# Kernel tuning notes

Hardware: AMD Instinct MI355X
Metric: run time of the kernel (lower is better)

The kernel has to match this reference:

```python
import jax, jax.numpy as jnp
import numpy as np

V = 50000        # output_size (vocab)
H = 1024         # internal hidden = hidden_size*2
L = 400          # max_length (encoder length)
B = 64
OOV_PAD = 500


def setup_inputs() -> dict:
    key = jax.random.key(0)
    ks = jax.random.split(key, 16)
    s = 0.02
    inp = {
        "input_ids": jax.random.randint(ks[0], (B,), 0, V),
        "hidden": jax.random.normal(ks[1], (1, B, H), jnp.float32),
        "encoder_outputs": jax.random.normal(ks[2], (L, B, H), jnp.float32),
        "full_input": jax.random.randint(ks[3], (B, L), 0, V),
        # parameters
        "emb": jax.random.normal(ks[4], (V, H), jnp.float32) * s,
        "attn_W": jax.random.normal(ks[5], (L, 2 * H), jnp.float32) * s,
        "attn_b": jnp.zeros((L,), jnp.float32),
        "comb_W": jax.random.normal(ks[6], (H, 2 * H), jnp.float32) * s,
        "comb_b": jnp.zeros((H,), jnp.float32),
        "W_ih": jax.random.normal(ks[7], (3 * H, H), jnp.float32) * s,
        "W_hh": jax.random.normal(ks[8], (3 * H, H), jnp.float32) * s,
        "b_ih": jnp.zeros((3 * H,), jnp.float32),
        "b_hh": jnp.zeros((3 * H,), jnp.float32),
        "out_W": jax.random.normal(ks[9], (V, H), jnp.float32) * s,
        "out_b": jnp.zeros((V,), jnp.float32),
        "gen_W": jax.random.normal(ks[10], (1, 2 * H), jnp.float32) * s,
        "gen_b": jnp.zeros((1,), jnp.float32),
    }
    return inp


def _decoder_step(input_ids, hidden, encoder_outputs, full_input,
                  emb, attn_W, attn_b, comb_W, comb_b,
                  W_ih, W_hh, b_ih, b_hh, out_W, out_b, gen_W, gen_b):
    embedded = emb[input_ids]                      # [B,H] (dropout is eval-mode identity)
    h0 = hidden[0]                                 # [B,H]

    # attention over fixed max_length positions
    cat = jnp.concatenate([embedded, h0], axis=1)  # [B,2H]
    attn_weights = jax.nn.softmax(cat @ attn_W.T + attn_b, axis=1)  # [B,L]
    enc = jnp.transpose(encoder_outputs, (1, 0, 2))                 # [B,L,H]
    attn_applied = jnp.einsum('bl,blh->bh', attn_weights, enc)      # [B,H]

    combined = jnp.concatenate([embedded, attn_applied], axis=1) @ comb_W.T + comb_b  # [B,H]

    # single-step GRU (PyTorch gate layout: r, z, n)
    gi = combined @ W_ih.T + b_ih
    gh = h0 @ W_hh.T + b_hh
    ir, iz, inn = jnp.split(gi, 3, axis=1)
    hr, hz, hn = jnp.split(gh, 3, axis=1)
    r = jax.nn.sigmoid(ir + hr)
    z = jax.nn.sigmoid(iz + hz)
    n = jnp.tanh(inn + r * hn)
    h_new = (1.0 - z) * n + z * h0                 # gru_output[0]

    p_vocab = jax.nn.log_softmax(h_new @ out_W.T + out_b, axis=1)   # [B,V]

    gen_in = jnp.concatenate([combined, h0], axis=1)                # [B,2H]
    p_gen = jax.nn.sigmoid(gen_in @ gen_W.T + gen_b)                # [B,1]

    # pointer copy distribution via scatter-add into [B, V+500]
    token_dist = jnp.zeros((input_ids.shape[0], V + OOV_PAD), p_vocab.dtype)
    rows = jnp.arange(input_ids.shape[0])[:, None]                  # [B,1]
    token_dist = token_dist.at[rows, full_input].add(attn_weights)

    p_vocab_scaled = p_vocab * p_gen
    padded = jnp.concatenate(
        [p_vocab_scaled, jnp.zeros((input_ids.shape[0], OOV_PAD), p_vocab.dtype)], axis=1)
    p_final = padded + (1.0 - p_gen) * token_dist
    # original module returns the INPUT hidden (not gru_hidden)
    return p_final, hidden, attn_weights


def reference(input_ids, hidden, encoder_outputs, full_input,
              emb, attn_W, attn_b, comb_W, comb_b,
              W_ih, W_hh, b_ih, b_hh, out_W, out_b, gen_W, gen_b):
    return _decoder_step(input_ids, hidden, encoder_outputs, full_input,
                         emb, attn_W, attn_b, comb_W, comb_b,
                         W_ih, W_hh, b_ih, b_hh, out_W, out_b, gen_W, gen_b)
```

## Files before the change

### kernel.cpp

```cpp
#include <hip/hip_runtime.h>
#include <cstddef>

#define B_ 64
#define H_ 1024
#define L_ 400
#define V_ 50000
#define VP_ 50500

typedef short short8 __attribute__((ext_vector_type(8)));
typedef float f32x4 __attribute__((ext_vector_type(4)));

static __device__ __forceinline__ short f2bf(float f) {
  unsigned u = __float_as_uint(f);
  u += 0x7fffu + ((u >> 16) & 1u);
  return (short)(u >> 16);
}

static __device__ __forceinline__ short8 pack8(float4 a, float4 b) {
  short8 r;
  r[0] = f2bf(a.x); r[1] = f2bf(a.y); r[2] = f2bf(a.z); r[3] = f2bf(a.w);
  r[4] = f2bf(b.x); r[5] = f2bf(b.y); r[6] = f2bf(b.z); r[7] = f2bf(b.w);
  return r;
}

__global__ void k_prep(const int* __restrict__ ids, const float* __restrict__ emb,
                       const float* __restrict__ hid, float* __restrict__ E,
                       float* __restrict__ A, float* __restrict__ hid_out) {
  int b = blockIdx.x;
  int t = threadIdx.x;
  int row = ids[b];
  float4 v = ((const float4*)(emb + (size_t)row * H_))[t];
  ((float4*)(E + (size_t)b * H_))[t] = v;
  ((float4*)(A + (size_t)b * H_))[t] = make_float4(0.f, 0.f, 0.f, 0.f);
  ((float4*)(hid_out + (size_t)b * H_))[t] = ((const float4*)(hid + (size_t)b * H_))[t];
}

__global__ __launch_bounds__(256) void k_gemm_small(
    const float* __restrict__ W0, const float* __restrict__ bias0,
    const float* __restrict__ Xa0, const float* __restrict__ Xb0,
    float* __restrict__ out0, int N0, int K0, int ldo0,
    const float* __restrict__ W1, const float* __restrict__ bias1,
    const float* __restrict__ Xa1, const float* __restrict__ Xb1,
    float* __restrict__ out1, int N1, int K1, int ldo1) {
  const float* W  = blockIdx.y ? W1  : W0;
  const float* bias = blockIdx.y ? bias1 : bias0;
  const float* Xa = blockIdx.y ? Xa1 : Xa0;
  const float* Xb = blockIdx.y ? Xb1 : Xb0;
  float* out = blockIdx.y ? out1 : out0;
  int N = blockIdx.y ? N1 : N0;
  int K = blockIdx.y ? K1 : K0;
  int ldo = blockIdx.y ? ldo1 : ldo0;

  int tid = threadIdx.x, wave = tid >> 6, lane = tid & 63;
  int q = lane >> 4, nl = lane & 15;
  int n = blockIdx.x * 16 + nl;
  int nld = n < N ? n : (N - 1);
  int kpw = K >> 2;
  int kbeg = wave * kpw;
  const float* wr = W + (size_t)nld * K;

  f32x4 acc[4];
  #pragma unroll
  for (int i = 0; i < 4; ++i) acc[i] = (f32x4){0.f, 0.f, 0.f, 0.f};

  for (int k0 = kbeg; k0 < kbeg + kpw; k0 += 32) {
    int kk = k0 + q * 8;
    float4 w0 = *(const float4*)(wr + kk);
    float4 w1 = *(const float4*)(wr + kk + 4);
    short8 bf = pack8(w0, w1);
    const float* Xsel = (kk < 1024) ? Xa : Xb;
    int kx = kk & 1023;
    #pragma unroll
    for (int mt = 0; mt < 4; ++mt) {
      const float* xp = Xsel + (size_t)(mt * 16 + nl) * H_ + kx;
      float4 x0 = *(const float4*)xp;
      float4 x1 = *(const float4*)(xp + 4);
      short8 af = pack8(x0, x1);
      acc[mt] = __builtin_amdgcn_mfma_f32_16x16x32_bf16(af, bf, acc[mt], 0, 0, 0);
    }
  }

  __shared__ float red[4][64][16];
  #pragma unroll
  for (int mt = 0; mt < 4; ++mt)
    #pragma unroll
    for (int r = 0; r < 4; ++r)
      red[wave][mt * 16 + q * 4 + r][nl] = acc[mt][r];
  __syncthreads();
  for (int i = tid; i < 1024; i += 256) {
    int m = i >> 4, c = i & 15;
    int nn = blockIdx.x * 16 + c;
    if (nn < N) {
      float s = red[0][m][c] + red[1][m][c] + red[2][m][c] + red[3][m][c] + bias[nn];
      out[(size_t)m * ldo + nn] = s;
    }
  }
}

__global__ __launch_bounds__(256) void k_attnsm(
    const float* __restrict__ S, const float* __restrict__ enc,
    float* __restrict__ aw_out, float* __restrict__ A) {
  __shared__ float w[L_];
  __shared__ float red[256];
  int lc = blockIdx.x, b = blockIdx.y, t = threadIdx.x;
  float a0 = S[b * L_ + t];
  float a1 = (t < L_ - 256) ? S[b * L_ + 256 + t] : -1e30f;
  float m = fmaxf(a0, a1);
  red[t] = m; __syncthreads();
  for (int s = 128; s > 0; s >>= 1) { if (t < s) red[t] = fmaxf(red[t], red[t + s]); __syncthreads(); }
  m = red[0]; __syncthreads();
  float e0 = __expf(a0 - m);
  float e1 = (t < L_ - 256) ? __expf(a1 - m) : 0.f;
  red[t] = e0 + e1; __syncthreads();
  for (int s = 128; s > 0; s >>= 1) { if (t < s) red[t] += red[t + s]; __syncthreads(); }
  float z = red[0];
  w[t] = e0 / z;
  if (t < L_ - 256) w[256 + t] = e1 / z;
  __syncthreads();
  if (lc == 0) {
    aw_out[b * L_ + t] = w[t];
    if (t < L_ - 256) aw_out[b * L_ + 256 + t] = w[256 + t];
  }
  float4 acc = make_float4(0.f, 0.f, 0.f, 0.f);
  for (int l = lc * 25; l < lc * 25 + 25; ++l) {
    float wg = w[l];
    float4 e = ((const float4*)(enc + ((size_t)l * B_ + b) * H_))[t];
    acc.x += wg * e.x; acc.y += wg * e.y; acc.z += wg * e.z; acc.w += wg * e.w;
  }
  float* dst = A + (size_t)b * H_ + t * 4;
  atomicAdd(dst + 0, acc.x); atomicAdd(dst + 1, acc.y);
  atomicAdd(dst + 2, acc.z); atomicAdd(dst + 3, acc.w);
}

__global__ __launch_bounds__(256) void k_gru_gen(
    const float* __restrict__ gi, const float* __restrict__ gh,
    const float* __restrict__ hid, short* __restrict__ HNb,
    const float* __restrict__ C, const float* __restrict__ gW,
    const float* __restrict__ gb, float* __restrict__ PG) {
  __shared__ float red[256];
  int blk = blockIdx.x, t = threadIdx.x;
  if (blk < 256) {
    int idx = blk * 256 + t;
    int b = idx >> 10, h = idx & 1023;
    float ir = gi[b * 3072 + h], iz = gi[b * 3072 + 1024 + h], inn = gi[b * 3072 + 2048 + h];
    float hr = gh[b * 3072 + h], hz = gh[b * 3072 + 1024 + h], hn = gh[b * 3072 + 2048 + h];
    float r = 1.f / (1.f + __expf(-(ir + hr)));
    float z = 1.f / (1.f + __expf(-(iz + hz)));
    float n = tanhf(inn + r * hn);
    HNb[idx] = f2bf((1.f - z) * n + z * hid[idx]);
  } else {
    int b = blk - 256;
    float acc = 0.f;
    for (int k = t; k < 2 * H_; k += 256) {
      float x = (k < H_) ? C[b * H_ + k] : hid[b * H_ + k - H_];
      acc += x * gW[k];
    }
    red[t] = acc; __syncthreads();
    for (int s = 128; s > 0; s >>= 1) { if (t < s) red[t] += red[t + s]; __syncthreads(); }
    if (t == 0) PG[b] = 1.f / (1.f + __expf(-(red[0] + gb[0])));
  }
}

__global__ __launch_bounds__(256) void k_gemm_vocab(
    const short* __restrict__ Xb, const float* __restrict__ W,
    const float* __restrict__ bias, float* __restrict__ P) {
  int tid = threadIdx.x, wave = tid >> 6, lane = tid & 63;
  int q = lane >> 4, nl = lane & 15;
  int n = blockIdx.x * 64 + wave * 16 + nl;
  int nld = n < V_ ? n : (V_ - 1);
  const float* wr = W + (size_t)nld * H_;
  f32x4 acc[4];
  #pragma unroll
  for (int i = 0; i < 4; ++i) acc[i] = (f32x4){0.f, 0.f, 0.f, 0.f};

  for (int k0 = 0; k0 < H_; k0 += 32) {
    int kk = k0 + q * 8;
    float4 w0 = *(const float4*)(wr + kk);
    float4 w1 = *(const float4*)(wr + kk + 4);
    short8 bf = pack8(w0, w1);
    #pragma unroll
    for (int mt = 0; mt < 4; ++mt) {
      short8 af = *(const short8*)(Xb + (size_t)(mt * 16 + nl) * H_ + kk);
      acc[mt] = __builtin_amdgcn_mfma_f32_16x16x32_bf16(af, bf, acc[mt], 0, 0, 0);
    }
  }
  if (n < V_) {
    float bv = bias[n];
    #pragma unroll
    for (int mt = 0; mt < 4; ++mt)
      #pragma unroll
      for (int r = 0; r < 4; ++r)
        P[(size_t)(mt * 16 + q * 4 + r) * VP_ + n] = acc[mt][r] + bv;
  }
}

__global__ __launch_bounds__(256) void k_rowred2(const float* __restrict__ P,
                                                 float* __restrict__ MX,
                                                 float* __restrict__ SE) {
  __shared__ float red[256];
  int b = blockIdx.x >> 2, c = blockIdx.x & 3;
  int t = threadIdx.x;
  int v0 = c * 12500, v1 = v0 + 12500;
  float m = -1e30f;
  for (int v = v0 + t; v < v1; v += 256) m = fmaxf(m, P[(size_t)b * VP_ + v]);
  red[t] = m; __syncthreads();
  for (int s = 128; s > 0; s >>= 1) { if (t < s) red[t] = fmaxf(red[t], red[t + s]); __syncthreads(); }
  m = red[0]; __syncthreads();
  float sum = 0.f;
  for (int v = v0 + t; v < v1; v += 256) sum += __expf(P[(size_t)b * VP_ + v] - m);
  red[t] = sum; __syncthreads();
  for (int s = 128; s > 0; s >>= 1) { if (t < s) red[t] += red[t + s]; __syncthreads(); }
  if (t == 0) { MX[blockIdx.x] = m; SE[blockIdx.x] = red[0]; }
}

__global__ void k_final(float* __restrict__ P, const float* __restrict__ pg,
                        const float* __restrict__ MX, const float* __restrict__ SE) {
  int b = blockIdx.y;
  float m0 = MX[b * 4], m1 = MX[b * 4 + 1], m2 = MX[b * 4 + 2], m3 = MX[b * 4 + 3];
  float M = fmaxf(fmaxf(m0, m1), fmaxf(m2, m3));
  float Z = SE[b * 4] * __expf(m0 - M) + SE[b * 4 + 1] * __expf(m1 - M)
          + SE[b * 4 + 2] * __expf(m2 - M) + SE[b * 4 + 3] * __expf(m3 - M);
  float lz = M + __logf(Z);
  float g = pg[b];
  int v0 = blockIdx.x * 1024 + threadIdx.x * 4;
  if (v0 >= VP_) return;
  float4* p = (float4*)(P + (size_t)b * VP_ + v0);
  if (v0 < V_) {
    float4 x = *p;
    x.x = g * (x.x - lz); x.y = g * (x.y - lz);
    x.z = g * (x.z - lz); x.w = g * (x.w - lz);
    *p = x;
  } else {
    *p = make_float4(0.f, 0.f, 0.f, 0.f);
  }
}

__global__ void k_scatter(float* __restrict__ P, const float* __restrict__ aw,
                          const int* __restrict__ fi, const float* __restrict__ pg) {
  int b = blockIdx.x, t = threadIdx.x;
  if (t >= L_) return;
  float g = 1.f - pg[b];
  int v = fi[b * L_ + t];
  atomicAdd(P + (size_t)b * VP_ + v, g * aw[b * L_ + t]);
}

extern "C" void kernel_launch(void* const* d_in, const int* in_sizes, int n_in,
                              void* d_out, int out_size, void* d_ws, size_t ws_size,
                              hipStream_t stream) {
  const int*   ids    = (const int*)d_in[0];
  const float* hid    = (const float*)d_in[1];
  const float* enc    = (const float*)d_in[2];
  const int*   fi     = (const int*)d_in[3];
  const float* emb    = (const float*)d_in[4];
  const float* attn_W = (const float*)d_in[5];
  const float* attn_b = (const float*)d_in[6];
  const float* comb_W = (const float*)d_in[7];
  const float* comb_b = (const float*)d_in[8];
  const float* W_ih   = (const float*)d_in[9];
  const float* W_hh   = (const float*)d_in[10];
  const float* b_ih   = (const float*)d_in[11];
  const float* b_hh   = (const float*)d_in[12];
  const float* out_W  = (const float*)d_in[13];
  const float* out_b  = (const float*)d_in[14];
  const float* gen_W  = (const float*)d_in[15];
  const float* gen_b  = (const float*)d_in[16];

  float* outp    = (float*)d_out;
  float* P       = outp;
  float* hid_out = outp + (size_t)B_ * VP_;
  float* aw_out  = hid_out + B_ * H_;

  float* ws = (float*)d_ws;
  float* E   = ws;
  float* A   = E + B_ * H_;
  float* C   = A + B_ * H_;
  float* S   = C + B_ * H_;
  float* GI  = S + B_ * L_;
  float* GH  = GI + B_ * 3 * H_;
  float* PG  = GH + B_ * 3 * H_;
  float* MX  = PG + B_;
  float* SE  = MX + 256;
  short* HNb = (short*)(SE + 256);

  k_prep<<<64, 256, 0, stream>>>(ids, emb, hid, E, A, hid_out);
  k_gemm_small<<<dim3(25, 1), 256, 0, stream>>>(
      attn_W, attn_b, E, hid, S, L_, 2 * H_, L_,
      attn_W, attn_b, E, hid, S, L_, 2 * H_, L_);
  k_attnsm<<<dim3(16, 64), 256, 0, stream>>>(S, enc, aw_out, A);
  k_gemm_small<<<dim3(64, 1), 256, 0, stream>>>(
      comb_W, comb_b, E, A, C, H_, 2 * H_, H_,
      comb_W, comb_b, E, A, C, H_, 2 * H_, H_);
  k_gemm_small<<<dim3(192, 2), 256, 0, stream>>>(
      W_ih, b_ih, C, C, GI, 3 * H_, H_, 3 * H_,
      W_hh, b_hh, hid, hid, GH, 3 * H_, H_, 3 * H_);
  k_gru_gen<<<320, 256, 0, stream>>>(GI, GH, hid, HNb, C, gen_W, gen_b, PG);
  k_gemm_vocab<<<782, 256, 0, stream>>>(HNb, out_W, out_b, P);
  k_rowred2<<<256, 256, 0, stream>>>(P, MX, SE);
  k_final<<<dim3(50, 64), 256, 0, stream>>>(P, PG, MX, SE);
  k_scatter<<<64, 512, 0, stream>>>(P, aw_out, fi, PG);
}
```

Baseline: 608.3 us.

## Fuse embedding gather, gate GEMMs, and row-max into fewer kernels

Drops the prep kernel by gathering embedding rows inside the attention/combine GEMMs. The attention-score and hidden-gate GEMMs now share one launch, and the generation gate runs in the input-gate GEMM launch. Attention application is split across hidden chunks with an in-block reduction instead of global atomics. The vocabulary GEMM emits per-block row maxima, so the softmax reduction no longer rescans logits for the max. This uses atomic sum accumulation and an extra workspace buffer.

```diff
diff --git a/kernel.cpp b/kernel.cpp
--- a/kernel.cpp
+++ b/kernel.cpp
@@ -6,6 +6,8 @@
 #define L_ 400
 #define V_ 50000
 #define VP_ 50500
+#define NBV_ 782
+#define BMXW_ 800
 
 typedef short short8 __attribute__((ext_vector_type(8)));
 typedef float f32x4 __attribute__((ext_vector_type(4)));
@@ -23,41 +25,47 @@
   return r;
 }
 
-__global__ void k_prep(const int* __restrict__ ids, const float* __restrict__ emb,
-                       const float* __restrict__ hid, float* __restrict__ E,
-                       float* __restrict__ A, float* __restrict__ hid_out) {
-  int b = blockIdx.x;
-  int t = threadIdx.x;
-  int row = ids[b];
-  float4 v = ((const float4*)(emb + (size_t)row * H_))[t];
-  ((float4*)(E + (size_t)b * H_))[t] = v;
-  ((float4*)(A + (size_t)b * H_))[t] = make_float4(0.f, 0.f, 0.f, 0.f);
-  ((float4*)(hid_out + (size_t)b * H_))[t] = ((const float4*)(hid + (size_t)b * H_))[t];
-}
-
-__global__ __launch_bounds__(256) void k_gemm_small(
-    const float* __restrict__ W0, const float* __restrict__ bias0,
-    const float* __restrict__ Xa0, const float* __restrict__ Xb0,
-    float* __restrict__ out0, int N0, int K0, int ldo0,
-    const float* __restrict__ W1, const float* __restrict__ bias1,
-    const float* __restrict__ Xa1, const float* __restrict__ Xb1,
-    float* __restrict__ out1, int N1, int K1, int ldo1) {
-  const float* W  = blockIdx.y ? W1  : W0;
-  const float* bias = blockIdx.y ? bias1 : bias0;
-  const float* Xa = blockIdx.y ? Xa1 : Xa0;
-  const float* Xb = blockIdx.y ? Xb1 : Xb0;
-  float* out = blockIdx.y ? out1 : out0;
-  int N = blockIdx.y ? N1 : N0;
-  int K = blockIdx.y ? K1 : K0;
-  int ldo = blockIdx.y ? ldo1 : ldo0;
-
-  int tid = threadIdx.x, wave = tid >> 6, lane = tid & 63;
+struct Job {
+  const float* W; const float* bias; const float* Xa; const float* Xb;
+  float* out; int N; int K; int ldo; int gather;
+};
+
+__global__ __launch_bounds__(256) void k_gemm2(
+    Job j0, int c0, Job j1, int c1,
+    const int* __restrict__ ids, const float* __restrict__ emb,
+    const float* __restrict__ pg_C, const float* __restrict__ pg_hid,
+    const float* __restrict__ gW, const float* __restrict__ gb,
+    float* __restrict__ PG) {
+  __shared__ float red[4][64][16];
+  __shared__ int sid[64];
+  __shared__ float redp[256];
+  int bid = blockIdx.x, tid = threadIdx.x;
+
+  if (bid >= c0 + c1) {
+    int b = bid - c0 - c1;
+    float acc = 0.f;
+    for (int k = tid; k < 2 * H_; k += 256) {
+      float x = (k < H_) ? pg_C[b * H_ + k] : pg_hid[b * H_ + k - H_];
+      acc += x * gW[k];
+    }
+    redp[tid] = acc; __syncthreads();
+    for (int s = 128; s > 0; s >>= 1) { if (tid < s) redp[tid] += redp[tid + s]; __syncthreads(); }
+    if (tid == 0) PG[b] = 1.f / (1.f + __expf(-(redp[0] + gb[0])));
+    return;
+  }
+
+  Job J = (bid < c0) ? j0 : j1;
+  int bx = (bid < c0) ? bid : bid - c0;
+  if (tid < 64) sid[tid] = ids[tid];
+  __syncthreads();
+
+  int wave = tid >> 6, lane = tid & 63;
   int q = lane >> 4, nl = lane & 15;
-  int n = blockIdx.x * 16 + nl;
-  int nld = n < N ? n : (N - 1);
-  int kpw = K >> 2;
+  int n = bx * 16 + nl;
+  int nld = n < J.N ? n : (J.N - 1);
+  int kpw = J.K >> 2;
   int kbeg = wave * kpw;
-  const float* wr = W + (size_t)nld * K;
+  const float* wr = J.W + (size_t)nld * J.K;
 
   f32x4 acc[4];
   #pragma unroll
@@ -68,11 +76,13 @@
     float4 w0 = *(const float4*)(wr + kk);
     float4 w1 = *(const float4*)(wr + kk + 4);
     short8 bf = pack8(w0, w1);
-    const float* Xsel = (kk < 1024) ? Xa : Xb;
-    int kx = kk & 1023;
     #pragma unroll
     for (int mt = 0; mt < 4; ++mt) {
-      const float* xp = Xsel + (size_t)(mt * 16 + nl) * H_ + kx;
+      int m = mt * 16 + nl;
+      const float* xp;
+      if (kk < H_) xp = (J.gather ? emb + (size_t)sid[m] * H_
+                                  : J.Xa + (size_t)m * H_) + kk;
+      else         xp = J.Xb + (size_t)m * H_ + (kk - H_);
       float4 x0 = *(const float4*)xp;
       float4 x1 = *(const float4*)(xp + 4);
       short8 af = pack8(x0, x1);
@@ -80,7 +90,6 @@
     }
   }
 
-  __shared__ float red[4][64][16];
   #pragma unroll
   for (int mt = 0; mt < 4; ++mt)
     #pragma unroll
@@ -88,21 +97,25 @@
       red[wave][mt * 16 + q * 4 + r][nl] = acc[mt][r];
   __syncthreads();
   for (int i = tid; i < 1024; i += 256) {
-    int m = i >> 4, c = i & 15;
-    int nn = blockIdx.x * 16 + c;
-    if (nn < N) {
-      float s = red[0][m][c] + red[1][m][c] + red[2][m][c] + red[3][m][c] + bias[nn];
-      out[(size_t)m * ldo + nn] = s;
-    }
-  }
-}
-
-__global__ __launch_bounds__(256) void k_attnsm(
+    int m = i >> 4, c2 = i & 15;
+    int nn = bx * 16 + c2;
+    if (nn < J.N) {
+      float s = red[0][m][c2] + red[1][m][c2] + red[2][m][c2] + red[3][m][c2] + J.bias[nn];
+      J.out[(size_t)m * J.ldo + nn] = s;
+    }
+  }
+}
+
+__global__ __launch_bounds__(256) void k_attnsm2(
     const float* __restrict__ S, const float* __restrict__ enc,
-    float* __restrict__ aw_out, float* __restrict__ A) {
+    float* __restrict__ aw_out, float* __restrict__ A,
+    const float* __restrict__ hid, float* __restrict__ hid_out,
+    float* __restrict__ SE64) {
   __shared__ float w[L_];
   __shared__ float red[256];
-  int lc = blockIdx.x, b = blockIdx.y, t = threadIdx.x;
+  __shared__ float4 rv[256];
+  int hc = blockIdx.x, b = blockIdx.y, t = threadIdx.x;
+
   float a0 = S[b * L_ + t];
   float a1 = (t < L_ - 256) ? S[b * L_ + 256 + t] : -1e30f;
   float m = fmaxf(a0, a1);
@@ -117,53 +130,54 @@
   w[t] = e0 / z;
   if (t < L_ - 256) w[256 + t] = e1 / z;
   __syncthreads();
-  if (lc == 0) {
+
+  if (hc == 8) {
     aw_out[b * L_ + t] = w[t];
     if (t < L_ - 256) aw_out[b * L_ + 256 + t] = w[256 + t];
-  }
+    ((float4*)(hid_out + (size_t)b * H_))[t] = ((const float4*)(hid + (size_t)b * H_))[t];
+    if (b == 0 && t < 64) SE64[t] = 0.f;
+    return;
+  }
+
+  int cq = t & 31, lg = t >> 5;
   float4 acc = make_float4(0.f, 0.f, 0.f, 0.f);
-  for (int l = lc * 25; l < lc * 25 + 25; ++l) {
+  const float* base = enc + (size_t)b * H_ + hc * 128 + cq * 4;
+  #pragma unroll 5
+  for (int l = lg; l < L_; l += 8) {
     float wg = w[l];
-    float4 e = ((const float4*)(enc + ((size_t)l * B_ + b) * H_))[t];
+    float4 e = *(const float4*)(base + (size_t)l * B_ * H_);
     acc.x += wg * e.x; acc.y += wg * e.y; acc.z += wg * e.z; acc.w += wg * e.w;
   }
-  float* dst = A + (size_t)b * H_ + t * 4;
-  atomicAdd(dst + 0, acc.x); atomicAdd(dst + 1, acc.y);
-  atomicAdd(dst + 2, acc.z); atomicAdd(dst + 3, acc.w);
-}
-
-__global__ __launch_bounds__(256) void k_gru_gen(
+  rv[t] = acc; __syncthreads();
+  if (t < 32) {
+    float4 s = rv[t];
+    #pragma unroll
+    for (int g = 1; g < 8; ++g) {
+      float4 o = rv[g * 32 + t];
+      s.x += o.x; s.y += o.y; s.z += o.z; s.w += o.w;
+    }
+    *(float4*)(A + (size_t)b * H_ + hc * 128 + t * 4) = s;
+  }
+}
+
+__global__ __launch_bounds__(256) void k_gru(
     const float* __restrict__ gi, const float* __restrict__ gh,
-    const float* __restrict__ hid, short* __restrict__ HNb,
-    const float* __restrict__ C, const float* __restrict__ gW,
-    const float* __restrict__ gb, float* __restrict__ PG) {
-  __shared__ float red[256];
-  int blk = blockIdx.x, t = threadIdx.x;
-  if (blk < 256) {
-    int idx = blk * 256 + t;
-    int b = idx >> 10, h = idx & 1023;
-    float ir = gi[b * 3072 + h], iz = gi[b * 3072 + 1024 + h], inn = gi[b * 3072 + 2048 + h];
-    float hr = gh[b * 3072 + h], hz = gh[b * 3072 + 1024 + h], hn = gh[b * 3072 + 2048 + h];
-    float r = 1.f / (1.f + __expf(-(ir + hr)));
-    float z = 1.f / (1.f + __expf(-(iz + hz)));
-    float n = tanhf(inn + r * hn);
-    HNb[idx] = f2bf((1.f - z) * n + z * hid[idx]);
-  } else {
-    int b = blk - 256;
-    float acc = 0.f;
-    for (int k = t; k < 2 * H_; k += 256) {
-      float x = (k < H_) ? C[b * H_ + k] : hid[b * H_ + k - H_];
-      acc += x * gW[k];
-    }
-    red[t] = acc; __syncthreads();
-    for (int s = 128; s > 0; s >>= 1) { if (t < s) red[t] += red[t + s]; __syncthreads(); }
-    if (t == 0) PG[b] = 1.f / (1.f + __expf(-(red[0] + gb[0])));
-  }
+    const float* __restrict__ hid, short* __restrict__ HNb) {
+  int idx = blockIdx.x * 256 + threadIdx.x;
+  int b = idx >> 10, h = idx & 1023;
+  float ir = gi[b * 3072 + h], iz = gi[b * 3072 + 1024 + h], inn = gi[b * 3072 + 2048 + h];
+  float hr = gh[b * 3072 + h], hz = gh[b * 3072 + 1024 + h], hn = gh[b * 3072 + 2048 + h];
+  float r = 1.f / (1.f + __expf(-(ir + hr)));
+  float z = 1.f / (1.f + __expf(-(iz + hz)));
+  float n = tanhf(inn + r * hn);
+  HNb[idx] = f2bf((1.f - z) * n + z * hid[idx]);
 }
 
 __global__ __launch_bounds__(256) void k_gemm_vocab(
     const short* __restrict__ Xb, const float* __restrict__ W,
-    const float* __restrict__ bias, float* __restrict__ P) {
+    const float* __restrict__ bias, float* __restrict__ P,
+    float* __restrict__ BMX) {
+  __shared__ float smax[4][64];
   int tid = threadIdx.x, wave = tid >> 6, lane = tid & 63;
   int q = lane >> 4, nl = lane & 15;
   int n = blockIdx.x * 64 + wave * 16 + nl;
@@ -184,43 +198,53 @@
       acc[mt] = __builtin_amdgcn_mfma_f32_16x16x32_bf16(af, bf, acc[mt], 0, 0, 0);
     }
   }
-  if (n < V_) {
-    float bv = bias[n];
-    #pragma unroll
-    for (int mt = 0; mt < 4; ++mt)
-      #pragma unroll
-      for (int r = 0; r < 4; ++r)
-        P[(size_t)(mt * 16 + q * 4 + r) * VP_ + n] = acc[mt][r] + bv;
-  }
-}
-
-__global__ __launch_bounds__(256) void k_rowred2(const float* __restrict__ P,
-                                                 float* __restrict__ MX,
-                                                 float* __restrict__ SE) {
+
+  float bv = (n < V_) ? bias[n] : 0.f;
+  #pragma unroll
+  for (int mt = 0; mt < 4; ++mt)
+    #pragma unroll
+    for (int r = 0; r < 4; ++r) {
+      float v = acc[mt][r] + bv;
+      if (n < V_) P[(size_t)(mt * 16 + q * 4 + r) * VP_ + n] = v;
+      float mx = (n < V_) ? v : -1e30f;
+      mx = fmaxf(mx, __shfl_xor(mx, 1));
+      mx = fmaxf(mx, __shfl_xor(mx, 2));
+      mx = fmaxf(mx, __shfl_xor(mx, 4));
+      mx = fmaxf(mx, __shfl_xor(mx, 8));
+      if (nl == 0) smax[wave][mt * 16 + q * 4 + r] = mx;
+    }
+  __syncthreads();
+  if (tid < 64) {
+    float m = fmaxf(fmaxf(smax[0][tid], smax[1][tid]),
+                    fmaxf(smax[2][tid], smax[3][tid]));
+    BMX[(size_t)tid * BMXW_ + blockIdx.x] = m;
+  }
+}
+
+__global__ __launch_bounds__(256) void k_sumexp(
+    const float* __restrict__ P, const float* __restrict__ BMX,
+    float* __restrict__ MXf, float* __restrict__ SE64) {
   __shared__ float red[256];
-  int b = blockIdx.x >> 2, c = blockIdx.x & 3;
-  int t = threadIdx.x;
-  int v0 = c * 12500, v1 = v0 + 12500;
+  int b = blockIdx.x >> 2, c = blockIdx.x & 3, t = threadIdx.x;
   float m = -1e30f;
-  for (int v = v0 + t; v < v1; v += 256) m = fmaxf(m, P[(size_t)b * VP_ + v]);
+  for (int i = t; i < NBV_; i += 256) m = fmaxf(m, BMX[(size_t)b * BMXW_ + i]);
   red[t] = m; __syncthreads();
   for (int s = 128; s > 0; s >>= 1) { if (t < s) red[t] = fmaxf(red[t], red[t + s]); __syncthreads(); }
   m = red[0]; __syncthreads();
+  if (c == 0 && t == 0) MXf[b] = m;
   float sum = 0.f;
-  for (int v = v0 + t; v < v1; v += 256) sum += __expf(P[(size_t)b * VP_ + v] - m);
+  int v0 = c * 12500;
+  for (int v = v0 + t; v < v0 + 12500; v += 256)
+    sum += __expf(P[(size_t)b * VP_ + v] - m);
   red[t] = sum; __syncthreads();
   for (int s = 128; s > 0; s >>= 1) { if (t < s) red[t] += red[t + s]; __syncthreads(); }
-  if (t == 0) { MX[blockIdx.x] = m; SE[blockIdx.x] = red[0]; }
+  if (t == 0) atomicAdd(SE64 + b, red[0]);
 }
 
 __global__ void k_final(float* __restrict__ P, const float* __restrict__ pg,
-                        const float* __restrict__ MX, const float* __restrict__ SE) {
+                        const float* __restrict__ MXf, const float* __restrict__ SE64) {
   int b = blockIdx.y;
-  float m0 = MX[b * 4], m1 = MX[b * 4 + 1], m2 = MX[b * 4 + 2], m3 = MX[b * 4 + 3];
-  float M = fmaxf(fmaxf(m0, m1), fmaxf(m2, m3));
-  float Z = SE[b * 4] * __expf(m0 - M) + SE[b * 4 + 1] * __expf(m1 - M)
-          + SE[b * 4 + 2] * __expf(m2 - M) + SE[b * 4 + 3] * __expf(m3 - M);
-  float lz = M + __logf(Z);
+  float lz = MXf[b] + __logf(SE64[b]);
   float g = pg[b];
   int v0 = blockIdx.x * 1024 + threadIdx.x * 4;
   if (v0 >= VP_) return;
@@ -271,31 +295,32 @@
   float* aw_out  = hid_out + B_ * H_;
 
   float* ws = (float*)d_ws;
-  float* E   = ws;
-  float* A   = E + B_ * H_;
-  float* C   = A + B_ * H_;
-  float* S   = C + B_ * H_;
-  float* GI  = S + B_ * L_;
-  float* GH  = GI + B_ * 3 * H_;
-  float* PG  = GH + B_ * 3 * H_;
-  float* MX  = PG + B_;
-  float* SE  = MX + 256;
-  short* HNb = (short*)(SE + 256);
-
-  k_prep<<<64, 256, 0, stream>>>(ids, emb, hid, E, A, hid_out);
-  k_gemm_small<<<dim3(25, 1), 256, 0, stream>>>(
-      attn_W, attn_b, E, hid, S, L_, 2 * H_, L_,
-      attn_W, attn_b, E, hid, S, L_, 2 * H_, L_);
-  k_attnsm<<<dim3(16, 64), 256, 0, stream>>>(S, enc, aw_out, A);
-  k_gemm_small<<<dim3(64, 1), 256, 0, stream>>>(
-      comb_W, comb_b, E, A, C, H_, 2 * H_, H_,
-      comb_W, comb_b, E, A, C, H_, 2 * H_, H_);
-  k_gemm_small<<<dim3(192, 2), 256, 0, stream>>>(
-      W_ih, b_ih, C, C, GI, 3 * H_, H_, 3 * H_,
-      W_hh, b_hh, hid, hid, GH, 3 * H_, H_, 3 * H_);
-  k_gru_gen<<<320, 256, 0, stream>>>(GI, GH, hid, HNb, C, gen_W, gen_b, PG);
-  k_gemm_vocab<<<782, 256, 0, stream>>>(HNb, out_W, out_b, P);
-  k_rowred2<<<256, 256, 0, stream>>>(P, MX, SE);
-  k_final<<<dim3(50, 64), 256, 0, stream>>>(P, PG, MX, SE);
+  float* A    = ws;
+  float* C    = A + B_ * H_;
+  float* S    = C + B_ * H_;
+  float* GI   = S + B_ * L_;
+  float* GH   = GI + B_ * 3 * H_;
+  float* PG   = GH + B_ * 3 * H_;
+  float* MXf  = PG + B_;
+  float* SE64 = MXf + B_;
+  float* BMX  = SE64 + B_;
+  short* HNb  = (short*)(BMX + B_ * BMXW_);
+
+  Job jattn = {attn_W, attn_b, emb, hid, S,  L_,     2 * H_, L_,     1};
+  Job jgh   = {W_hh,   b_hh,   hid, hid, GH, 3 * H_, H_,     3 * H_, 0};
+  Job jcomb = {comb_W, comb_b, emb, A,   C,  H_,     2 * H_, H_,     1};
+  Job jgi   = {W_ih,   b_ih,   C,   C,   GI, 3 * H_, H_,     3 * H_, 0};
+
+  k_gemm2<<<217, 256, 0, stream>>>(jattn, 25, jgh, 192,
+      ids, emb, C, hid, gen_W, gen_b, PG);
+  k_attnsm2<<<dim3(9, 64), 256, 0, stream>>>(S, enc, aw_out, A, hid, hid_out, SE64);
+  k_gemm2<<<64, 256, 0, stream>>>(jcomb, 64, jcomb, 0,
+      ids, emb, C, hid, gen_W, gen_b, PG);
+  k_gemm2<<<256, 256, 0, stream>>>(jgi, 192, jgi, 0,
+      ids, emb, C, hid, gen_W, gen_b, PG);
+  k_gru<<<256, 256, 0, stream>>>(GI, GH, hid, HNb);
+  k_gemm_vocab<<<NBV_, 256, 0, stream>>>(HNb, out_W, out_b, P, BMX);
+  k_sumexp<<<256, 256, 0, stream>>>(P, BMX, MXf, SE64);
+  k_final<<<dim3(50, 64), 256, 0, stream>>>(P, PG, MXf, SE64);
   k_scatter<<<64, 512, 0, stream>>>(P, aw_out, fi, PG);
 }
```

Result: slower. 644.2 us (+5.9%).
